# Kernel optimization log

Measured on AMD Instinct MI355X. Metric: run time of the kernel, lower is better.

## Reference

```python
import jax, jax.numpy as jnp
import numpy as np

EMBED_DIM = 1024
NUM_HEADS = 16
HEAD_DIM = EMBED_DIM // NUM_HEADS


def setup_inputs() -> dict:
    key = jax.random.key(0)
    ks = jax.random.split(key, 9)
    B, S, D = 2, 2048, EMBED_DIM
    scale = 1.0 / np.sqrt(D)
    x = jax.random.normal(ks[0], (B, S, D), dtype=jnp.float32)
    # nn.Linear weights are stored as (out, in); y = x @ W.T + b
    Wq = jax.random.uniform(ks[1], (D, D), jnp.float32, -scale, scale)
    bq = jax.random.uniform(ks[2], (D,), jnp.float32, -scale, scale)
    Wk = jax.random.uniform(ks[3], (D, D), jnp.float32, -scale, scale)
    bk = jax.random.uniform(ks[4], (D,), jnp.float32, -scale, scale)
    Wv = jax.random.uniform(ks[5], (D, D), jnp.float32, -scale, scale)
    bv = jax.random.uniform(ks[6], (D,), jnp.float32, -scale, scale)
    Wo = jax.random.uniform(ks[7], (D, D), jnp.float32, -scale, scale)
    bo = jax.random.uniform(ks[8], (D,), jnp.float32, -scale, scale)
    return {"x": x, "Wq": Wq, "bq": bq, "Wk": Wk, "bk": bk,
            "Wv": Wv, "bv": bv, "Wo": Wo, "bo": bo}


def reference(x, Wq, bq, Wk, bk, Wv, bv, Wo, bo):
    B, S, D = x.shape
    H, Hd = NUM_HEADS, HEAD_DIM

    def split_heads(t):  # [B,S,D] -> [B,H,S,Hd]
        return t.reshape(B, S, H, Hd).transpose(0, 2, 1, 3)

    Q = split_heads(x @ Wq.T + bq)
    K = split_heads(x @ Wk.T + bk)
    V = split_heads(x @ Wv.T + bv)

    scores = jnp.einsum('bhqd,bhkd->bhqk', Q, K) / jnp.sqrt(
        jnp.asarray(Hd, dtype=x.dtype))
    attn = jax.nn.softmax(scores, axis=-1)
    out = jnp.einsum('bhqk,bhkd->bhqd', attn, V)  # [B,H,S,Hd]
    out = out.transpose(0, 2, 1, 3).reshape(B, S, D)
    return out @ Wo.T + bo
```

## Files before the change

### kernel.cpp

```cpp
#include <hip/hip_runtime.h>
#include <hip/hip_bf16.h>
#include <stdint.h>

typedef __attribute__((ext_vector_type(8))) short short8;
typedef __attribute__((ext_vector_type(4))) float f32x4;
typedef unsigned short u16;
typedef unsigned int u32;

static constexpr int S = 2048;
static constexpr int H = 16;
static constexpr int HD = 64;

__device__ __forceinline__ float fast_exp2(float x){
  return __builtin_amdgcn_exp2f(x);
}

__device__ __forceinline__ u16 f2bf(float f){
  union { float f; u32 u; } x; x.f = f;
  u32 r = x.u + 0x7fffu + ((x.u >> 16) & 1u);
  return (u16)(r >> 16);
}

__device__ __forceinline__ u32 cvt_pk_bf16(float lo, float hi){
  u32 r;
  asm("v_cvt_pk_bf16_f32 %0, %1, %2" : "=v"(r) : "v"(lo), "v"(hi));
  return r;
}

__global__ __launch_bounds__(256) void cast_f32_bf16(const float* __restrict__ src,
                                                     u16* __restrict__ dst, int n){
  int i = (blockIdx.x * 256 + threadIdx.x) * 4;
  if (i >= n) return;
  float4 v = *(const float4*)(src + i);
  ushort4 o;
  o.x = f2bf(v.x); o.y = f2bf(v.y); o.z = f2bf(v.z); o.w = f2bf(v.w);
  *(ushort4*)(dst + i) = o;
}

__global__ __launch_bounds__(256) void cast_w4(const float* __restrict__ a,
                                               const float* __restrict__ b,
                                               const float* __restrict__ c,
                                               const float* __restrict__ d,
                                               u16* __restrict__ dst){
  int i = (blockIdx.x * 256 + threadIdx.x) * 4;
  const float* s = (i < 2097152) ? ((i < 1048576) ? a : b)
                                 : ((i < 3145728) ? c : d);
  float4 v = *(const float4*)(s + (i & 1048575));
  ushort4 o;
  o.x = f2bf(v.x); o.y = f2bf(v.y); o.z = f2bf(v.z); o.w = f2bf(v.w);
  *(ushort4*)(dst + i) = o;
}

__device__ __forceinline__ void gload_lds16(const void* g, void* lds_uniform){
  __builtin_amdgcn_global_load_lds(
      (const __attribute__((address_space(1))) u32*)g,
      (__attribute__((address_space(3))) u32*)lds_uniform,
      16, 0, 0);
}

template<int EPI>
__global__ __launch_bounds__(256) void gemm_bt(const u16* __restrict__ A,
                                               const u16* __restrict__ Wall,
                                               const float* __restrict__ b0p,
                                               const float* __restrict__ b1p,
                                               const float* __restrict__ b2p,
                                               u16* __restrict__ obf,
                                               float* __restrict__ ofp){
  __shared__ __align__(16) u16 As[128*32];
  __shared__ __align__(16) u16 Bs[128*32];

  const int tid  = threadIdx.x;
  const int lane = tid & 63;
  const int wid  = tid >> 6;
  const int wm = wid >> 1, wn = wid & 1;
  const int l4 = lane >> 4, l15 = lane & 15;

  int m0, n0, z;
  if (EPI == 0){
    const int L = blockIdx.x + 8*blockIdx.y + 256*blockIdx.z;
    const int W = (L & 7)*96 + (L >> 3);
    z = W >> 8;
    const int rem = W & 255;
    n0 = (rem & 7) * 128;
    m0 = (rem >> 3) * 128;
  } else {
    const int L = blockIdx.x + 8*blockIdx.y;
    const int W = (L & 7)*32 + (L >> 3);
    z = 0;
    n0 = (W & 7) * 128;
    m0 = (W >> 3) * 128;
  }

  const u16* Bw = Wall + (size_t)z * (1024*1024);
  const float* bias = (z == 0) ? b0p : ((z == 1) ? b1p : b2p);

  f32x4 acc[4][4];
  #pragma unroll
  for (int m=0;m<4;m++)
    #pragma unroll
    for (int n=0;n<4;n++) acc[m][n] = (f32x4){0.f,0.f,0.f,0.f};

  const char* Ab = (const char*)A  + (size_t)m0 * 2048;
  const char* Bb = (const char*)Bw + (size_t)n0 * 2048;
  char* AsB = (char*)As;
  char* BsB = (char*)Bs;

  int ldsu[2], row_[2], col_[2];
  #pragma unroll
  for (int p=0;p<2;p++){
    ldsu[p] = wid*1024 + p*4096;
    int b = ldsu[p] + lane*16;
    row_[p] = b >> 6;
    col_[p] = b & 63;
  }

  for (int kt = 0; kt < 32; ++kt){
    const int kb = kt * 64;
    #pragma unroll
    for (int p=0;p<2;p++){
      gload_lds16(Ab + (size_t)row_[p]*2048 + kb + col_[p], AsB + ldsu[p]);
      gload_lds16(Bb + (size_t)row_[p]*2048 + kb + col_[p], BsB + ldsu[p]);
    }
    __syncthreads();

    short8 af[4], bfr[4];
    const int kcol = 8 * l4;
    #pragma unroll
    for (int m=0;m<4;m++)
      af[m] = *(const short8*)&As[(wm*64 + m*16 + l15)*32 + kcol];
    #pragma unroll
    for (int n=0;n<4;n++)
      bfr[n] = *(const short8*)&Bs[(wn*64 + n*16 + l15)*32 + kcol];

    #pragma unroll
    for (int m=0;m<4;m++)
      #pragma unroll
      for (int n=0;n<4;n++)
        acc[m][n] = __builtin_amdgcn_mfma_f32_16x16x32_bf16(af[m], bfr[n], acc[m][n], 0,0,0);

    __syncthreads();
  }

  #pragma unroll
  for (int m=0;m<4;m++){
    const int rgb = m0 + wm*64 + m*16 + 4*l4;
    #pragma unroll
    for (int n=0;n<4;n++){
      const int cg = n0 + wn*64 + n*16 + l15;
      const float bb = bias[cg];
      if (EPI == 0){
        const int bi = rgb >> 11, si = rgb & 2047;
        const int hi = cg >> 6,  hd = cg & 63;
        if (z == 2){
          u16* outz = obf + (size_t)2 * 4194304u;
          ushort4 o;
          o.x = f2bf(acc[m][n][0] + bb);
          o.y = f2bf(acc[m][n][1] + bb);
          o.z = f2bf(acc[m][n][2] + bb);
          o.w = f2bf(acc[m][n][3] + bb);
          *(ushort4*)&outz[(((size_t)(bi*16 + hi))*64 + hd)*2048 + si] = o;
        } else {
          u16* outz = obf + (size_t)z * 4194304u;
          const float sc = (z == 0) ? 0.18033688011112042f : 1.0f;
          #pragma unroll
          for (int r=0;r<4;r++)
            outz[(((size_t)(bi*16 + hi))*2048 + (si + r))*64 + hd] =
                f2bf((acc[m][n][r] + bb) * sc);
        }
      } else {
        #pragma unroll
        for (int r=0;r<4;r++)
          ofp[(size_t)(rgb + r)*1024 + cg] = acc[m][n][r] + bb;
      }
    }
  }
}

__global__ __launch_bounds__(256) void attn_fwd(const u16* __restrict__ Qg,
                                                const u16* __restrict__ Kg,
                                                const u16* __restrict__ Vtg,
                                                u16* __restrict__ Og){
  __shared__ __align__(16) u16 Ks[2*64*64];
  __shared__ __align__(16) u16 Vs[2*64*64];
  __shared__ __align__(16) u16 Ps[4*2*16*64];

  const int tid  = threadIdx.x;
  const int lane = tid & 63;
  const int wid  = tid >> 6;
  const int l4 = lane >> 4, l15 = lane & 15;
  const int swz = l15 & 7;

  const int L = blockIdx.x + 16*blockIdx.y;
  const int W = (L & 7)*64 + (L >> 3);
  const int qb = W & 15;
  const int bh = W >> 4;
  const size_t hoff = (size_t)bh * (S * HD);

  short8 aq[2][2];
  #pragma unroll
  for (int g=0; g<2; ++g){
    const u16* qp = Qg + hoff + (size_t)(qb*128 + wid*32 + g*16 + l15) * HD;
    aq[g][0] = *(const short8*)(qp + 8*l4);
    aq[g][1] = *(const short8*)(qp + 32 + 8*l4);
  }

  float mr[2] = {-1e30f, -1e30f};
  float lr[2] = {0.f, 0.f};
  f32x4 oacc[2][4];
  #pragma unroll
  for (int g=0; g<2; ++g)
    #pragma unroll
    for (int hb=0;hb<4;hb++) oacc[g][hb] = (f32x4){0.f,0.f,0.f,0.f};

  const char* Kb = (const char*)(Kg  + hoff);
  const char* Vb = (const char*)(Vtg + hoff);
  char* KsB = (char*)Ks;
  char* VsB = (char*)Vs;
  char* PsB = (char*)Ps + wid*4096;

  int ldsu[2], srcK[2], srcV[2];
  #pragma unroll
  for (int p=0;p<2;p++){
    ldsu[p] = wid*2048 + p*1024;
    int b   = ldsu[p] + lane*16;
    int row = b >> 7, cc = (b >> 4) & 7;
    int ccs = cc ^ (row & 7);
    srcK[p] = row*128  + (ccs << 4);
    srcV[p] = row*4096 + (ccs << 4);
  }

  #pragma unroll
  for (int p=0;p<2;p++){
    gload_lds16(Kb + srcK[p], KsB + ldsu[p]);
    gload_lds16(Vb + srcV[p], VsB + ldsu[p]);
  }
  __syncthreads();

  #pragma unroll 2
  for (int kt = 0; kt < S/64; ++kt){
    const int cur = kt & 1;
    if (kt + 1 < S/64){
      const int nxt = cur ^ 1;
      const char* Ksrc = Kb + (size_t)(kt+1)*8192;
      const char* Vsrc = Vb + (size_t)(kt+1)*128;
      #pragma unroll
      for (int p=0;p<2;p++){
        gload_lds16(Ksrc + srcK[p], KsB + nxt*8192 + ldsu[p]);
        gload_lds16(Vsrc + srcV[p], VsB + nxt*8192 + ldsu[p]);
      }
    }

    const char* KsC = KsB + cur*8192;
    const char* VsC = VsB + cur*8192;

    f32x4 sacc[2][4];
    __builtin_amdgcn_s_setprio(1);
    #pragma unroll
    for (int nb=0;nb<4;nb++){
      const int krow = nb*16 + l15;
      short8 k0 = *(const short8*)(KsC + krow*128 + ((l4 ^ swz) << 4));
      short8 k1 = *(const short8*)(KsC + krow*128 + (((4 + l4) ^ swz) << 4));
      #pragma unroll
      for (int g=0; g<2; ++g){
        f32x4 zz = (f32x4){0.f,0.f,0.f,0.f};
        zz = __builtin_amdgcn_mfma_f32_16x16x32_bf16(k0, aq[g][0], zz, 0,0,0);
        zz = __builtin_amdgcn_mfma_f32_16x16x32_bf16(k1, aq[g][1], zz, 0,0,0);
        sacc[g][nb] = zz;
      }
    }
    __builtin_amdgcn_s_setprio(0);

    #pragma unroll
    for (int g=0; g<2; ++g){
      float t0 = fmaxf(fmaxf(sacc[g][0][0], sacc[g][0][1]), fmaxf(sacc[g][0][2], sacc[g][0][3]));
      float t1 = fmaxf(fmaxf(sacc[g][1][0], sacc[g][1][1]), fmaxf(sacc[g][1][2], sacc[g][1][3]));
      float t2 = fmaxf(fmaxf(sacc[g][2][0], sacc[g][2][1]), fmaxf(sacc[g][2][2], sacc[g][2][3]));
      float t3 = fmaxf(fmaxf(sacc[g][3][0], sacc[g][3][1]), fmaxf(sacc[g][3][2], sacc[g][3][3]));
      float t = fmaxf(fmaxf(t0, t1), fmaxf(t2, t3));

      if (!__all(t <= mr[g] + 8.f)){
        float tw = fmaxf(t, __shfl_xor(t, 16, 64));
        tw = fmaxf(tw, __shfl_xor(tw, 32, 64));
        const float mnew = fmaxf(mr[g], tw);
        const float alpha = fast_exp2(mr[g] - mnew);
        mr[g] = mnew;
        lr[g] *= alpha;
        float af[4];
        #pragma unroll
        for (int r=0;r<4;r++) af[r] = __shfl(alpha, 4*l4 + r, 64);
        #pragma unroll
        for (int hb=0;hb<4;hb++)
          #pragma unroll
          for (int r=0;r<4;r++) oacc[g][hb][r] *= af[r];
      }

      float rs = 0.f;
      #pragma unroll
      for (int nb=0;nb<4;nb++)
        #pragma unroll
        for (int r=0;r<4;r++){
          float p = fast_exp2(sacc[g][nb][r] - mr[g]);
          sacc[g][nb][r] = p;
          rs += p;
        }
      lr[g] += rs;

      #pragma unroll
      for (int nb=0;nb<4;nb++){
        u32 lo = cvt_pk_bf16(sacc[g][nb][0], sacc[g][nb][1]);
        u32 hi = cvt_pk_bf16(sacc[g][nb][2], sacc[g][nb][3]);
        const int chunk = nb*2 + (l4 >> 1);
        const int sub   = (l4 & 1) * 8;
        *(uint2*)(PsB + g*2048 + l15*128 + ((chunk ^ swz) << 4) + sub) = make_uint2(lo, hi);
      }
    }

    __builtin_amdgcn_s_setprio(1);
    #pragma unroll
    for (int ks=0;ks<2;ks++){
      short8 ap0 = *(const short8*)(PsB +        l15*128 + (((ks*4 + l4) ^ swz) << 4));
      short8 ap1 = *(const short8*)(PsB + 2048 + l15*128 + (((ks*4 + l4) ^ swz) << 4));
      #pragma unroll
      for (int hb=0;hb<4;hb++){
        const int vrow = hb*16 + l15;
        short8 bv = *(const short8*)(VsC + vrow*128 + (((ks*4 + l4) ^ swz) << 4));
        oacc[0][hb] = __builtin_amdgcn_mfma_f32_16x16x32_bf16(ap0, bv, oacc[0][hb], 0,0,0);
        oacc[1][hb] = __builtin_amdgcn_mfma_f32_16x16x32_bf16(ap1, bv, oacc[1][hb], 0,0,0);
      }
    }
    __builtin_amdgcn_s_setprio(0);
    __syncthreads();
  }

  const int b = bh >> 4, h = bh & 15;
  #pragma unroll
  for (int g=0; g<2; ++g){
    float lg = lr[g];
    lg += __shfl_xor(lg, 16, 64);
    lg += __shfl_xor(lg, 32, 64);
    float inv[4];
    #pragma unroll
    for (int r=0;r<4;r++){
      float lq = __shfl(lg, 4*l4 + r, 64);
      inv[r] = 1.0f / lq;
    }
    #pragma unroll
    for (int hb=0;hb<4;hb++){
      #pragma unroll
      for (int r=0;r<4;r++){
        const int si = qb*128 + wid*32 + g*16 + 4*l4 + r;
        const float v = oacc[g][hb][r] * inv[r];
        Og[(((size_t)(b*S + si))*H + h)*HD + hb*16 + l15] = f2bf(v);
      }
    }
  }
}

extern "C" void kernel_launch(void* const* d_in, const int* in_sizes, int n_in,
                              void* d_out, int out_size, void* d_ws, size_t ws_size,
                              hipStream_t stream) {
  const float* x  = (const float*)d_in[0];
  const float* Wq = (const float*)d_in[1];
  const float* bq = (const float*)d_in[2];
  const float* Wk = (const float*)d_in[3];
  const float* bk = (const float*)d_in[4];
  const float* Wv = (const float*)d_in[5];
  const float* bv = (const float*)d_in[6];
  const float* Wo = (const float*)d_in[7];
  const float* bo = (const float*)d_in[8];

  char* ws = (char*)d_ws;
  u16* xb  = (u16*)(ws);
  u16* Wb  = (u16*)(ws + (size_t)8*1024*1024);
  u16* QKV = (u16*)(ws + (size_t)16*1024*1024);
  u16* AO  = (u16*)(ws + (size_t)40*1024*1024);
  float* out = (float*)d_out;

  cast_f32_bf16<<<4096, 256, 0, stream>>>(x, xb, 4194304);
  cast_w4<<<4096, 256, 0, stream>>>(Wq, Wk, Wv, Wo, Wb);

  dim3 g1(8, 32, 3);
  gemm_bt<0><<<g1, 256, 0, stream>>>(xb, Wb, bq, bk, bv, QKV, nullptr);

  dim3 g2(16, 32, 1);
  attn_fwd<<<g2, 256, 0, stream>>>(QKV, QKV + 4194304, QKV + 2*4194304, AO);

  dim3 g3(8, 32, 1);
  gemm_bt<1><<<g3, 256, 0, stream>>>(AO, Wb + 3145728, bo, bo, bo, nullptr, out);
}
```

Before: 138.9 us.

## Halve attention block to two waves over 64 queries and fuse cast kernels

The attention kernel now runs 128-thread blocks of 2 waves covering 64 query rows, doubling the grid to 1024 blocks. Each wave issues twice as many K/V async LDS loads to fill the shared tiles. Separately, the x cast and the four weight casts are merged into one launch. The aim is better CU occupancy and load balance, plus one fewer launch. The cost is that each K/V tile loaded into LDS is reused by fewer queries, which raises global/L2 traffic for K and V.

```diff
diff --git a/kernel.cpp b/kernel.cpp
--- a/kernel.cpp
+++ b/kernel.cpp
@@ -27,28 +27,28 @@
   return r;
 }
 
-__global__ __launch_bounds__(256) void cast_f32_bf16(const float* __restrict__ src,
-                                                     u16* __restrict__ dst, int n){
+__global__ __launch_bounds__(256) void cast_all(const float* __restrict__ x,
+                                                const float* __restrict__ Wq,
+                                                const float* __restrict__ Wk,
+                                                const float* __restrict__ Wv,
+                                                const float* __restrict__ Wo,
+                                                u16* __restrict__ xb,
+                                                u16* __restrict__ Wb){
   int i = (blockIdx.x * 256 + threadIdx.x) * 4;
-  if (i >= n) return;
-  float4 v = *(const float4*)(src + i);
+  const float* s; u16* d; int off;
+  if (i < 4194304){
+    s = x; d = xb; off = i;
+  } else {
+    int j = i - 4194304;
+    int w = j >> 20;
+    s = (w == 0) ? Wq : (w == 1) ? Wk : (w == 2) ? Wv : Wo;
+    d = Wb + (w << 20);
+    off = j & 1048575;
+  }
+  float4 v = *(const float4*)(s + off);
   ushort4 o;
   o.x = f2bf(v.x); o.y = f2bf(v.y); o.z = f2bf(v.z); o.w = f2bf(v.w);
-  *(ushort4*)(dst + i) = o;
-}
-
-__global__ __launch_bounds__(256) void cast_w4(const float* __restrict__ a,
-                                               const float* __restrict__ b,
-                                               const float* __restrict__ c,
-                                               const float* __restrict__ d,
-                                               u16* __restrict__ dst){
-  int i = (blockIdx.x * 256 + threadIdx.x) * 4;
-  const float* s = (i < 2097152) ? ((i < 1048576) ? a : b)
-                                 : ((i < 3145728) ? c : d);
-  float4 v = *(const float4*)(s + (i & 1048575));
-  ushort4 o;
-  o.x = f2bf(v.x); o.y = f2bf(v.y); o.z = f2bf(v.z); o.w = f2bf(v.w);
-  *(ushort4*)(dst + i) = o;
+  *(ushort4*)(d + off) = o;
 }
 
 __device__ __forceinline__ void gload_lds16(const void* g, void* lds_uniform){
@@ -176,13 +176,13 @@
   }
 }
 
-__global__ __launch_bounds__(256) void attn_fwd(const u16* __restrict__ Qg,
+__global__ __launch_bounds__(128) void attn_fwd(const u16* __restrict__ Qg,
                                                 const u16* __restrict__ Kg,
                                                 const u16* __restrict__ Vtg,
                                                 u16* __restrict__ Og){
   __shared__ __align__(16) u16 Ks[2*64*64];
   __shared__ __align__(16) u16 Vs[2*64*64];
-  __shared__ __align__(16) u16 Ps[4*2*16*64];
+  __shared__ __align__(16) u16 Ps[2*2*16*64];
 
   const int tid  = threadIdx.x;
   const int lane = tid & 63;
@@ -190,16 +190,16 @@
   const int l4 = lane >> 4, l15 = lane & 15;
   const int swz = l15 & 7;
 
-  const int L = blockIdx.x + 16*blockIdx.y;
-  const int W = (L & 7)*64 + (L >> 3);
-  const int qb = W & 15;
-  const int bh = W >> 4;
+  const int L = blockIdx.x + 32*blockIdx.y;
+  const int W = (L & 7)*128 + (L >> 3);
+  const int qb = W & 31;
+  const int bh = W >> 5;
   const size_t hoff = (size_t)bh * (S * HD);
 
   short8 aq[2][2];
   #pragma unroll
   for (int g=0; g<2; ++g){
-    const u16* qp = Qg + hoff + (size_t)(qb*128 + wid*32 + g*16 + l15) * HD;
+    const u16* qp = Qg + hoff + (size_t)(qb*64 + wid*32 + g*16 + l15) * HD;
     aq[g][0] = *(const short8*)(qp + 8*l4);
     aq[g][1] = *(const short8*)(qp + 32 + 8*l4);
   }
@@ -218,10 +218,10 @@
   char* VsB = (char*)Vs;
   char* PsB = (char*)Ps + wid*4096;
 
-  int ldsu[2], srcK[2], srcV[2];
-  #pragma unroll
-  for (int p=0;p<2;p++){
-    ldsu[p] = wid*2048 + p*1024;
+  int ldsu[4], srcK[4], srcV[4];
+  #pragma unroll
+  for (int p=0;p<4;p++){
+    ldsu[p] = wid*1024 + p*2048;
     int b   = ldsu[p] + lane*16;
     int row = b >> 7, cc = (b >> 4) & 7;
     int ccs = cc ^ (row & 7);
@@ -230,7 +230,7 @@
   }
 
   #pragma unroll
-  for (int p=0;p<2;p++){
+  for (int p=0;p<4;p++){
     gload_lds16(Kb + srcK[p], KsB + ldsu[p]);
     gload_lds16(Vb + srcV[p], VsB + ldsu[p]);
   }
@@ -244,7 +244,7 @@
       const char* Ksrc = Kb + (size_t)(kt+1)*8192;
       const char* Vsrc = Vb + (size_t)(kt+1)*128;
       #pragma unroll
-      for (int p=0;p<2;p++){
+      for (int p=0;p<4;p++){
         gload_lds16(Ksrc + srcK[p], KsB + nxt*8192 + ldsu[p]);
         gload_lds16(Vsrc + srcV[p], VsB + nxt*8192 + ldsu[p]);
       }
@@ -348,7 +348,7 @@
     for (int hb=0;hb<4;hb++){
       #pragma unroll
       for (int r=0;r<4;r++){
-        const int si = qb*128 + wid*32 + g*16 + 4*l4 + r;
+        const int si = qb*64 + wid*32 + g*16 + 4*l4 + r;
         const float v = oacc[g][hb][r] * inv[r];
         Og[(((size_t)(b*S + si))*H + h)*HD + hb*16 + l15] = f2bf(v);
       }
@@ -376,14 +376,13 @@
   u16* AO  = (u16*)(ws + (size_t)40*1024*1024);
   float* out = (float*)d_out;
 
-  cast_f32_bf16<<<4096, 256, 0, stream>>>(x, xb, 4194304);
-  cast_w4<<<4096, 256, 0, stream>>>(Wq, Wk, Wv, Wo, Wb);
+  cast_all<<<8192, 256, 0, stream>>>(x, Wq, Wk, Wv, Wo, xb, Wb);
 
   dim3 g1(8, 32, 3);
   gemm_bt<0><<<g1, 256, 0, stream>>>(xb, Wb, bq, bk, bv, QKV, nullptr);
 
-  dim3 g2(16, 32, 1);
-  attn_fwd<<<g2, 256, 0, stream>>>(QKV, QKV + 4194304, QKV + 2*4194304, AO);
+  dim3 g2(32, 32, 1);
+  attn_fwd<<<g2, 128, 0, stream>>>(QKV, QKV + 4194304, QKV + 2*4194304, AO);
 
   dim3 g3(8, 32, 1);
   gemm_bt<1><<<g3, 256, 0, stream>>>(AO, Wb + 3145728, bo, bo, bo, nullptr, out);
```

Result: slower. 142.5 us (+2.6%).
